# Optimization experiments

Measured on AMD Instinct MI355X. Metric: run time of the kernel, lower is better.

## Reference

```python
import jax, jax.numpy as jnp
import numpy as np

B = 16          # batch_size
N = 100000      # num_nodes (neurons)
E = 2000000     # num_edges (synapses)
D = 512         # decision-making nodes (decision_making_vector.sum())
C = 10          # num classes
NUM_PASSES = 4  # NUM_CONNECTOME_PASSES


def setup_inputs() -> dict:
    key = jax.random.key(0)
    ks = jax.random.split(key, 8)
    x = jax.random.normal(ks[0], (B * N, 1), dtype=jnp.float32)
    edge_weight = jax.random.normal(ks[1], (E,), dtype=jnp.float32)
    edge_weight_multiplier = jax.random.uniform(ks[2], (E,), minval=-1.0, maxval=1.0, dtype=jnp.float32)
    neuron_threshold = jax.random.uniform(ks[3], (N,), minval=0.0, maxval=0.1, dtype=jnp.float32)
    fc_w = jax.random.normal(ks[4], (C, D), dtype=jnp.float32) / np.float32(np.sqrt(D))
    fc_b = jnp.zeros((C,), jnp.float32)
    edge_index = jax.random.randint(ks[5], (2, E), 0, N, dtype=jnp.int32)
    decision_indices = jnp.sort(jax.random.randint(ks[6], (D,), 0, N, dtype=jnp.int32))
    return {
        "x": x,
        "edge_weight": edge_weight,
        "edge_weight_multiplier": edge_weight_multiplier,
        "neuron_threshold": neuron_threshold,
        "fc_w": fc_w,
        "fc_b": fc_b,
        "edge_index": edge_index,
        "decision_indices": decision_indices,
    }


def reference(x, edge_weight, edge_weight_multiplier, neuron_threshold, fc_w, fc_b,
              edge_index, decision_indices):
    xb = x.reshape(B, N)                      # per-graph neuron activations
    src, dst = edge_index[0], edge_index[1]
    # message weights: edge_weight * tanh(multiplier)  (train_edges, not refined)
    w = edge_weight * jnp.tanh(edge_weight_multiplier)   # [E]
    thr = jnp.abs(neuron_threshold)                      # [N]
    for _ in range(NUM_PASSES):
        msg = xb[:, src] * w                              # gather + mul, [B, E]
        aggr = jnp.zeros_like(xb).at[:, dst].add(msg)     # scatter-add, [B, N]
        amin, amax = aggr.min(), aggr.max()               # global min-max norm
        xb = jax.nn.sigmoid((aggr - amin) / (amax - amin) - thr)  # lambda_func update
    xd = xb[:, decision_indices]                          # decision-making mask, [B, D]
    # final_layer == 'nn', train_neurons -> no norm; eval dropout = identity
    return xd @ fc_w.T + fc_b                             # [B, C]
```

## Files before the change

kernel.cpp:

```cpp
#include <hip/hip_runtime.h>

#define Bsz 16
#define Nn  100000
#define Ee  2000000
#define Dd  512
#define Cc  10
#define NB  (Nn * Bsz)
#define NB4 (NB / 4)
#define NPARTS ((NB4 + 255) / 256)
#define NBK 196
#define BPAD 16
#define BE   4096
#define SEDMAX 12288

__device__ __forceinline__ unsigned enc_f(float f) {
    unsigned u = __float_as_uint(f);
    return (u & 0x80000000u) ? ~u : (u | 0x80000000u);
}
__device__ __forceinline__ float dec_f(unsigned e) {
    unsigned u = (e & 0x80000000u) ? (e ^ 0x80000000u) : ~e;
    return __uint_as_float(u);
}
__device__ __forceinline__ unsigned short tob(float f) {
    unsigned u = __float_as_uint(f);
    return (unsigned short)((u + 0x7FFFu + ((u >> 16) & 1u)) >> 16);
}
__device__ __forceinline__ float tof(unsigned short h) {
    return __uint_as_float((unsigned)h << 16);
}

__global__ void prep(const float* __restrict__ x, const float* __restrict__ nt,
                     unsigned short* __restrict__ xh, float* __restrict__ thr,
                     int* __restrict__ bcnt) {
    __shared__ float sm[16][65];
    int t = threadIdx.x;
    int n0 = blockIdx.x * 64;
    #pragma unroll
    for (int rep = 0; rep < 4; rep++) {
        int r = rep * 4 + (t >> 6);
        int c = t & 63;
        int n = n0 + c;
        sm[r][c] = (n < Nn) ? x[r * Nn + n] : 0.0f;
    }
    __syncthreads();
    int nn = t >> 2, bq = t & 3;
    int n = n0 + nn;
    if (n < Nn) {
        ushort4 h;
        h.x = tob(sm[bq * 4 + 0][nn]);
        h.y = tob(sm[bq * 4 + 1][nn]);
        h.z = tob(sm[bq * 4 + 2][nn]);
        h.w = tob(sm[bq * 4 + 3][nn]);
        ((ushort4*)xh)[n * 4 + bq] = h;
    }
    int gid = blockIdx.x * 256 + t;
    if (gid < Nn) thr[gid] = fabsf(nt[gid]);
    if (gid < NBK) bcnt[gid] = 0;
}

__global__ void bhist(const int* __restrict__ dstv, int* __restrict__ bcnt) {
    __shared__ int lh[NBK];
    int t = threadIdx.x;
    if (t < NBK) lh[t] = 0;
    __syncthreads();
    int e = blockIdx.x * BE + t;
    #pragma unroll
    for (int j = 0; j < BE / 256; j++, e += 256)
        if (e < Ee) atomicAdd(&lh[dstv[e] >> 9], 1);
    __syncthreads();
    if (t < NBK && lh[t] > 0) atomicAdd(&bcnt[t], lh[t]);
}

__global__ void bscan(const int* __restrict__ bcnt, int* __restrict__ bbase,
                      int* __restrict__ bcur) {
    __shared__ int s[256];
    int t = threadIdx.x;
    int v = (t < NBK) ? bcnt[t] : 0;
    s[t] = v;
    __syncthreads();
    for (int off = 1; off < 256; off <<= 1) {
        int u = (t >= off) ? s[t - off] : 0;
        __syncthreads();
        s[t] += u;
        __syncthreads();
    }
    if (t < NBK) {
        int excl = s[t] - v;
        bbase[t] = excl;
        bcur[t * BPAD] = excl;
    }
    if (t == 0) bbase[NBK] = Ee;
}

__global__ void bin1(const int* __restrict__ srcv, const int* __restrict__ dstv,
                     const float* __restrict__ ew, const float* __restrict__ mult,
                     int* __restrict__ bcur, int2* __restrict__ csr_sw) {
    __shared__ int2  sdat[BE];
    __shared__ short sbk[BE];
    __shared__ int   sbase[NBK];
    __shared__ int   scur[NBK];
    __shared__ int   sg[NBK];
    __shared__ int   ss[256];
    int t = threadIdx.x;
    int e0 = blockIdx.x * BE;
    if (t < NBK) scur[t] = 0;
    __syncthreads();
    #pragma unroll
    for (int j = 0; j < BE / 256; j++) {
        int e = e0 + t + j * 256;
        if (e < Ee) atomicAdd(&scur[dstv[e] >> 9], 1);
    }
    __syncthreads();
    int v = (t < NBK) ? scur[t] : 0;
    ss[t] = v;
    __syncthreads();
    for (int off = 1; off < 256; off <<= 1) {
        int u = (t >= off) ? ss[t - off] : 0;
        __syncthreads();
        ss[t] += u;
        __syncthreads();
    }
    int excl = ss[t] - v;
    if (t < NBK) {
        if (v > 0) sg[t] = atomicAdd(&bcur[t * BPAD], v);
        sbase[t] = excl;
        scur[t]  = excl;
    }
    __syncthreads();
    #pragma unroll
    for (int j = 0; j < BE / 256; j++) {
        int e = e0 + t + j * 256;
        if (e < Ee) {
            int d = dstv[e];
            int bk = d >> 9;
            int pos = atomicAdd(&scur[bk], 1);
            int2 p;
            p.x = srcv[e] | ((d & 511) << 17);
            p.y = __float_as_int(ew[e] * tanhf(mult[e]));
            sdat[pos] = p;
            sbk[pos] = (short)bk;
        }
    }
    __syncthreads();
    int cnt = min(Ee - e0, BE);
    for (int s = t; s < cnt; s += 256) {
        int bk = sbk[s];
        csr_sw[sg[bk] + (s - sbase[bk])] = sdat[s];
    }
}

__global__ __launch_bounds__(512) void bin2(const int* __restrict__ bbase,
                                            int2* __restrict__ csr_sw,
                                            int* __restrict__ row) {
    __shared__ int2 sed[SEDMAX];
    __shared__ int  lh[512];
    __shared__ int  lscan[512];
    int b = blockIdx.x;
    int n0 = b * 512;
    int n1 = min(n0 + 512, Nn);
    int e0 = bbase[b], e1 = bbase[b + 1];
    int cnt = e1 - e0;
    if (cnt > SEDMAX) cnt = SEDMAX;
    int t = threadIdx.x;
    lh[t] = 0;
    for (int s = t; s < cnt; s += 512) sed[s] = csr_sw[e0 + s];
    __syncthreads();
    for (int s = t; s < cnt; s += 512) atomicAdd(&lh[(sed[s].x >> 17) & 511], 1);
    __syncthreads();
    int v = lh[t];
    lscan[t] = v;
    __syncthreads();
    for (int off = 1; off < 512; off <<= 1) {
        int u = (t >= off) ? lscan[t - off] : 0;
        __syncthreads();
        lscan[t] += u;
        __syncthreads();
    }
    int excl = lscan[t] - v;
    int n = n0 + t;
    if (n < n1) row[n] = e0 + excl;
    if (b == NBK - 1 && t == 0) row[Nn] = Ee;
    lh[t] = excl;
    __syncthreads();
    for (int s = t; s < cnt; s += 512) {
        int2 p = sed[s];
        int nl = (p.x >> 17) & 511;
        int pos = atomicAdd(&lh[nl], 1);
        csr_sw[e0 + pos] = make_int2(p.x & 0x1FFFF, p.y);
    }
}

__global__ void gather(const int* __restrict__ row, const int2* __restrict__ csr_sw,
                       const unsigned short* __restrict__ xh, float* __restrict__ aggr,
                       uint2* __restrict__ part) {
    int i = blockIdx.x * 256 + threadIdx.x;
    bool active = i < NB4;
    float4 acc = make_float4(0.f, 0.f, 0.f, 0.f);
    if (active) {
        int n = i >> 2, bq = i & 3;
        int ks = row[n], ke = row[n + 1];
        const ushort4* x4 = (const ushort4*)xh;
        for (int k = ks; k < ke; k += 8) {
            int2    p[8];
            ushort4 v[8];
            #pragma unroll
            for (int j = 0; j < 8; ++j) {
                int kk = k + j;
                int kc = kk < ke ? kk : ks;
                p[j] = csr_sw[kc];
                if (kk >= ke) p[j].y = 0;
            }
            #pragma unroll
            for (int j = 0; j < 8; ++j) v[j] = x4[p[j].x * 4 + bq];
            #pragma unroll
            for (int j = 0; j < 8; ++j) {
                float w = __int_as_float(p[j].y);
                acc.x += tof(v[j].x) * w;
                acc.y += tof(v[j].y) * w;
                acc.z += tof(v[j].z) * w;
                acc.w += tof(v[j].w) * w;
            }
        }
        ((float4*)aggr)[i] = acc;
    }

    float lmin = active ? fminf(fminf(acc.x, acc.y), fminf(acc.z, acc.w)) : INFINITY;
    float lmax = active ? fmaxf(fmaxf(acc.x, acc.y), fmaxf(acc.z, acc.w)) : -INFINITY;
    #pragma unroll
    for (int off = 32; off > 0; off >>= 1) {
        lmin = fminf(lmin, __shfl_down(lmin, off));
        lmax = fmaxf(lmax, __shfl_down(lmax, off));
    }
    __shared__ float smin[4], smax[4];
    int wid = threadIdx.x >> 6, lane = threadIdx.x & 63;
    if (lane == 0) { smin[wid] = lmin; smax[wid] = lmax; }
    __syncthreads();
    if (threadIdx.x == 0) {
        float m0 = smin[0], M0 = smax[0];
        #pragma unroll
        for (int k = 1; k < 4; k++) { m0 = fminf(m0, smin[k]); M0 = fmaxf(M0, smax[k]); }
        part[blockIdx.x] = make_uint2(enc_f(m0), enc_f(M0));
    }
}

__global__ void mm_reduce(const uint2* __restrict__ part, unsigned* __restrict__ mm) {
    unsigned lmin = 0xFFFFFFFFu, lmax = 0u;
    for (int i = threadIdx.x; i < NPARTS; i += 1024) {
        uint2 p = part[i];
        lmin = min(lmin, p.x);
        lmax = max(lmax, p.y);
    }
    #pragma unroll
    for (int off = 32; off > 0; off >>= 1) {
        lmin = min(lmin, __shfl_down(lmin, off));
        lmax = max(lmax, __shfl_down(lmax, off));
    }
    __shared__ unsigned smn[16], smx[16];
    int wid = threadIdx.x >> 6, lane = threadIdx.x & 63;
    if (lane == 0) { smn[wid] = lmin; smx[wid] = lmax; }
    __syncthreads();
    if (threadIdx.x == 0) {
        #pragma unroll
        for (int k = 1; k < 16; k++) { lmin = min(lmin, smn[k]); lmax = max(lmax, smx[k]); }
        mm[0] = lmin;
        mm[1] = lmax;
    }
}

__global__ void update(float* __restrict__ aggr, const float* __restrict__ thr,
                       const unsigned* __restrict__ mm, unsigned short* __restrict__ xh,
                       int last) {
    int q = blockIdx.x * blockDim.x + threadIdx.x;
    if (q < NB4) {
        float amin = dec_f(mm[0]), amax = dec_f(mm[1]);
        float inv = 1.0f / (amax - amin);
        int n = q >> 2;
        float t = thr[n];
        float4 a = ((const float4*)aggr)[q];
        float4 r;
        r.x = 1.0f / (1.0f + expf(-((a.x - amin) * inv - t)));
        r.y = 1.0f / (1.0f + expf(-((a.y - amin) * inv - t)));
        r.z = 1.0f / (1.0f + expf(-((a.z - amin) * inv - t)));
        r.w = 1.0f / (1.0f + expf(-((a.w - amin) * inv - t)));
        if (last) {
            ((float4*)aggr)[q] = r;
        } else {
            ushort4 h;
            h.x = tob(r.x); h.y = tob(r.y); h.z = tob(r.z); h.w = tob(r.w);
            ((ushort4*)xh)[q] = h;
        }
    }
}

__global__ void final_k(const float* __restrict__ xf, const int* __restrict__ dix,
                        const float* __restrict__ fcw, const float* __restrict__ fcb,
                        float* __restrict__ out) {
    __shared__ float xd[Dd][Bsz];
    int j = threadIdx.x;
    int n = dix[j];
    #pragma unroll
    for (int b = 0; b < Bsz; b++) xd[j][b] = xf[n * 16 + b];
    __syncthreads();
    if (j < Bsz * Cc) {
        int b = j / Cc, c = j % Cc;
        float acc = fcb[c];
        for (int k = 0; k < Dd; k++) acc += xd[k][b] * fcw[c * Dd + k];
        out[b * Cc + c] = acc;
    }
}

extern "C" void kernel_launch(void* const* d_in, const int* in_sizes, int n_in,
                              void* d_out, int out_size, void* d_ws, size_t ws_size,
                              hipStream_t stream) {
    const float* x    = (const float*)d_in[0];
    const float* ew   = (const float*)d_in[1];
    const float* mult = (const float*)d_in[2];
    const float* nt   = (const float*)d_in[3];
    const float* fcw  = (const float*)d_in[4];
    const float* fcb  = (const float*)d_in[5];
    const int*   ei   = (const int*)d_in[6];
    const int*   dix  = (const int*)d_in[7];
    float* out = (float*)d_out;

    const int* srcv = ei;
    const int* dstv = ei + Ee;

    unsigned short* xh = (unsigned short*)d_ws;
    float* aggr    = (float*)(xh + NB);
    float* thr     = aggr + NB;
    int2*  csr_sw  = (int2*)(thr + Nn);
    uint2* part    = (uint2*)(csr_sw + Ee);
    int*   row     = (int*)(part + NPARTS);
    int*   bcnt    = row + Nn + 1;
    int*   bbase   = bcnt + NBK;
    int*   bcur    = bbase + NBK + 1;
    unsigned* mm   = (unsigned*)(bcur + NBK * BPAD);

    prep<<<(Nn + 63) / 64, 256, 0, stream>>>(x, nt, xh, thr, bcnt);
    bhist<<<(Ee + BE - 1) / BE, 256, 0, stream>>>(dstv, bcnt);
    bscan<<<1, 256, 0, stream>>>(bcnt, bbase, bcur);
    bin1<<<(Ee + BE - 1) / BE, 256, 0, stream>>>(srcv, dstv, ew, mult, bcur, csr_sw);
    bin2<<<NBK, 512, 0, stream>>>(bbase, csr_sw, row);

    for (int p = 0; p < 4; p++) {
        gather<<<NPARTS, 256, 0, stream>>>(row, csr_sw, xh, aggr, part);
        mm_reduce<<<1, 1024, 0, stream>>>(part, mm);
        update<<<(NB4 + 255) / 256, 256, 0, stream>>>(aggr, thr, mm, xh, p == 3);
    }

    final_k<<<1, 512, 0, stream>>>(aggr, dix, fcw, fcb, out);
}
```

Before: 292.9 us.

## Gather 8 batches per thread and fold min-max reduction into gather

Each gather thread now handles 8 batch lanes of a node instead of 4, so every CSR edge entry is read by 2 threads rather than 4, and the source activations are loaded as 16-byte vectors. The separate single-block mm_reduce launch is removed. The last gather block to finish, detected through an atomic counter and thread fences, reduces the per-block partial min/max and resets the counter. This cuts edge-index traffic and one launch per pass, at the cost of half as many threads (less latency hiding) and more registers per thread.

```diff
diff --git a/kernel.cpp b/kernel.cpp
--- a/kernel.cpp
+++ b/kernel.cpp
@@ -7,12 +7,15 @@
 #define Cc  10
 #define NB  (Nn * Bsz)
 #define NB4 (NB / 4)
-#define NPARTS ((NB4 + 255) / 256)
+#define NB8 (NB / 8)
+#define NP2 ((NB8 + 255) / 256)
 #define NBK 196
 #define BPAD 16
 #define BE   4096
 #define SEDMAX 12288
 
+typedef unsigned short us8 __attribute__((ext_vector_type(8)));
+
 __device__ __forceinline__ unsigned enc_f(float f) {
     unsigned u = __float_as_uint(f);
     return (u & 0x80000000u) ? ~u : (u | 0x80000000u);
@@ -31,7 +34,7 @@
 
 __global__ void prep(const float* __restrict__ x, const float* __restrict__ nt,
                      unsigned short* __restrict__ xh, float* __restrict__ thr,
-                     int* __restrict__ bcnt) {
+                     int* __restrict__ bcnt, int* __restrict__ ctr) {
     __shared__ float sm[16][65];
     int t = threadIdx.x;
     int n0 = blockIdx.x * 64;
@@ -56,6 +59,7 @@
     int gid = blockIdx.x * 256 + t;
     if (gid < Nn) thr[gid] = fabsf(nt[gid]);
     if (gid < NBK) bcnt[gid] = 0;
+    if (gid == 0) *ctr = 0;
 }
 
 __global__ void bhist(const int* __restrict__ dstv, int* __restrict__ bcnt) {
@@ -192,17 +196,20 @@
 
 __global__ void gather(const int* __restrict__ row, const int2* __restrict__ csr_sw,
                        const unsigned short* __restrict__ xh, float* __restrict__ aggr,
-                       uint2* __restrict__ part) {
+                       uint2* __restrict__ part, unsigned* __restrict__ mm,
+                       int* __restrict__ ctr) {
     int i = blockIdx.x * 256 + threadIdx.x;
-    bool active = i < NB4;
-    float4 acc = make_float4(0.f, 0.f, 0.f, 0.f);
+    bool active = i < NB8;
+    float acc[8];
+    #pragma unroll
+    for (int b = 0; b < 8; b++) acc[b] = 0.0f;
     if (active) {
-        int n = i >> 2, bq = i & 3;
+        int n = i >> 1, h = i & 1;
         int ks = row[n], ke = row[n + 1];
-        const ushort4* x4 = (const ushort4*)xh;
+        const us8* x8 = (const us8*)xh;
         for (int k = ks; k < ke; k += 8) {
-            int2    p[8];
-            ushort4 v[8];
+            int2 p[8];
+            us8  v[8];
             #pragma unroll
             for (int j = 0; j < 8; ++j) {
                 int kk = k + j;
@@ -211,27 +218,35 @@
                 if (kk >= ke) p[j].y = 0;
             }
             #pragma unroll
-            for (int j = 0; j < 8; ++j) v[j] = x4[p[j].x * 4 + bq];
+            for (int j = 0; j < 8; ++j) v[j] = x8[p[j].x * 2 + h];
             #pragma unroll
             for (int j = 0; j < 8; ++j) {
                 float w = __int_as_float(p[j].y);
-                acc.x += tof(v[j].x) * w;
-                acc.y += tof(v[j].y) * w;
-                acc.z += tof(v[j].z) * w;
-                acc.w += tof(v[j].w) * w;
+                #pragma unroll
+                for (int b = 0; b < 8; b++) acc[b] += tof(v[j][b]) * w;
             }
         }
-        ((float4*)aggr)[i] = acc;
-    }
-
-    float lmin = active ? fminf(fminf(acc.x, acc.y), fminf(acc.z, acc.w)) : INFINITY;
-    float lmax = active ? fmaxf(fmaxf(acc.x, acc.y), fmaxf(acc.z, acc.w)) : -INFINITY;
+        float4 o0 = make_float4(acc[0], acc[1], acc[2], acc[3]);
+        float4 o1 = make_float4(acc[4], acc[5], acc[6], acc[7]);
+        ((float4*)aggr)[i * 2]     = o0;
+        ((float4*)aggr)[i * 2 + 1] = o1;
+    }
+
+    float lmin = INFINITY, lmax = -INFINITY;
+    if (active) {
+        #pragma unroll
+        for (int b = 0; b < 8; b++) {
+            lmin = fminf(lmin, acc[b]);
+            lmax = fmaxf(lmax, acc[b]);
+        }
+    }
     #pragma unroll
     for (int off = 32; off > 0; off >>= 1) {
         lmin = fminf(lmin, __shfl_down(lmin, off));
         lmax = fmaxf(lmax, __shfl_down(lmax, off));
     }
     __shared__ float smin[4], smax[4];
+    __shared__ int isLast;
     int wid = threadIdx.x >> 6, lane = threadIdx.x & 63;
     if (lane == 0) { smin[wid] = lmin; smax[wid] = lmax; }
     __syncthreads();
@@ -240,30 +255,34 @@
         #pragma unroll
         for (int k = 1; k < 4; k++) { m0 = fminf(m0, smin[k]); M0 = fmaxf(M0, smax[k]); }
         part[blockIdx.x] = make_uint2(enc_f(m0), enc_f(M0));
-    }
-}
-
-__global__ void mm_reduce(const uint2* __restrict__ part, unsigned* __restrict__ mm) {
-    unsigned lmin = 0xFFFFFFFFu, lmax = 0u;
-    for (int i = threadIdx.x; i < NPARTS; i += 1024) {
-        uint2 p = part[i];
-        lmin = min(lmin, p.x);
-        lmax = max(lmax, p.y);
-    }
-    #pragma unroll
-    for (int off = 32; off > 0; off >>= 1) {
-        lmin = min(lmin, __shfl_down(lmin, off));
-        lmax = max(lmax, __shfl_down(lmax, off));
-    }
-    __shared__ unsigned smn[16], smx[16];
-    int wid = threadIdx.x >> 6, lane = threadIdx.x & 63;
-    if (lane == 0) { smn[wid] = lmin; smx[wid] = lmax; }
-    __syncthreads();
-    if (threadIdx.x == 0) {
+        __threadfence();
+        int c = atomicAdd(ctr, 1);
+        isLast = (c == (int)gridDim.x - 1);
+    }
+    __syncthreads();
+    if (isLast) {
+        __threadfence();
+        unsigned umin = 0xFFFFFFFFu, umax = 0u;
+        for (int s = threadIdx.x; s < NP2; s += 256) {
+            uint2 p = part[s];
+            umin = min(umin, p.x);
+            umax = max(umax, p.y);
+        }
         #pragma unroll
-        for (int k = 1; k < 16; k++) { lmin = min(lmin, smn[k]); lmax = max(lmax, smx[k]); }
-        mm[0] = lmin;
-        mm[1] = lmax;
+        for (int off = 32; off > 0; off >>= 1) {
+            umin = min(umin, __shfl_down(umin, off));
+            umax = max(umax, __shfl_down(umax, off));
+        }
+        __shared__ unsigned smn[4], smx[4];
+        if (lane == 0) { smn[wid] = umin; smx[wid] = umax; }
+        __syncthreads();
+        if (threadIdx.x == 0) {
+            #pragma unroll
+            for (int k = 1; k < 4; k++) { umin = min(umin, smn[k]); umax = max(umax, smx[k]); }
+            mm[0] = umin;
+            mm[1] = umax;
+            *ctr = 0;
+        }
     }
 }
 
@@ -330,21 +349,21 @@
     float* thr     = aggr + NB;
     int2*  csr_sw  = (int2*)(thr + Nn);
     uint2* part    = (uint2*)(csr_sw + Ee);
-    int*   row     = (int*)(part + NPARTS);
+    int*   row     = (int*)(part + NP2);
     int*   bcnt    = row + Nn + 1;
     int*   bbase   = bcnt + NBK;
     int*   bcur    = bbase + NBK + 1;
-    unsigned* mm   = (unsigned*)(bcur + NBK * BPAD);
-
-    prep<<<(Nn + 63) / 64, 256, 0, stream>>>(x, nt, xh, thr, bcnt);
+    int*   ctr     = bcur + NBK * BPAD;
+    unsigned* mm   = (unsigned*)(ctr + 1);
+
+    prep<<<(Nn + 63) / 64, 256, 0, stream>>>(x, nt, xh, thr, bcnt, ctr);
     bhist<<<(Ee + BE - 1) / BE, 256, 0, stream>>>(dstv, bcnt);
     bscan<<<1, 256, 0, stream>>>(bcnt, bbase, bcur);
     bin1<<<(Ee + BE - 1) / BE, 256, 0, stream>>>(srcv, dstv, ew, mult, bcur, csr_sw);
     bin2<<<NBK, 512, 0, stream>>>(bbase, csr_sw, row);
 
     for (int p = 0; p < 4; p++) {
-        gather<<<NPARTS, 256, 0, stream>>>(row, csr_sw, xh, aggr, part);
-        mm_reduce<<<1, 1024, 0, stream>>>(part, mm);
+        gather<<<NP2, 256, 0, stream>>>(row, csr_sw, xh, aggr, part, mm, ctr);
         update<<<(NB4 + 255) / 256, 256, 0, stream>>>(aggr, thr, mm, xh, p == 3);
     }
 
```

Measured after the change: 407.3 us. +39.1%, slower.
